# Kernel optimization log

Hardware: AMD Instinct MI355X
Metric: run time of the kernel (lower is better)

The kernel has to match this reference:

```python
import jax, jax.numpy as jnp
import numpy as np

B, D, R = 16384, 4096, 64       # batch tokens, embed_dim, low_rank_dimension
N_PART = 8                       # number of subspace partitions
P = R // N_PART                  # partition size = 8
N_SEL = 4                        # partitions selected per example


def setup_inputs() -> dict:
    key = jax.random.key(0)
    k1, k2, k3, k4 = jax.random.split(key, 4)
    base = jax.random.normal(k1, (B, D), dtype=jnp.float32)
    source = jax.random.normal(k2, (B, D), dtype=jnp.float32)
    # orthogonal low-rank rotation (torch.nn.utils.parametrizations.orthogonal)
    W, _ = jnp.linalg.qr(jax.random.normal(k3, (D, R), dtype=jnp.float32))  # [D, R], orthonormal cols
    subspaces = jax.random.randint(k4, (B, N_SEL), 0, N_PART)               # partition ids per example
    return {"base": base, "source": source, "W": W, "subspaces": subspaces}


def reference(base, source, W, subspaces):
    # rotate into low-rank space: [B, R]
    rotated_base = base @ W
    rotated_source = source @ W
    diff = rotated_source - rotated_base

    # per-example selected rotated-space indices (contiguous partitions of size P)
    # idx[b] = concat over selected partitions of [p*P, p*P+P)
    idx = (subspaces[:, :, None] * P + jnp.arange(P)).reshape(B, N_SEL * P)  # [B, N_SEL*P]

    # Selecting columns of diff and matching rows of W.T, then matmul, is
    # equivalent to masking unselected rotated dims to zero and doing one GEMM.
    mask = jnp.zeros((B, R), dtype=diff.dtype).at[jnp.arange(B)[:, None], idx].set(1.0)
    output = base + (diff * mask) @ W.T  # [B, D]
    return output.astype(base.dtype)
```

## Files before the change

kernel.cpp:

```cpp
#include <hip/hip_runtime.h>


#define D_DIM 4096
#define R_DIM 64
#define BM    32
#define WAVESTG 16384
#define OFF_RM  65536
#define SMEM_BYTES 70144

typedef short bf16vec8 __attribute__((ext_vector_type(8)));
typedef float f32x4v  __attribute__((ext_vector_type(4)));

__device__ __forceinline__ unsigned int f2bf_u(float f) {
  unsigned int u = __builtin_bit_cast(unsigned int, f);
  return (u + 0x7fffu + ((u >> 16) & 1u)) >> 16;
}
__device__ __forceinline__ unsigned int pack2bf(float a, float b) {
  return f2bf_u(a) | (f2bf_u(b) << 16);
}
__device__ __forceinline__ void async_ld16(const void* g, void* l) {
  __builtin_amdgcn_global_load_lds(
      (const __attribute__((address_space(1))) void*)g,
      (__attribute__((address_space(3))) void*)l, 16, 0, 0);
}

__global__ __launch_bounds__(256)
void lrri_prep(const float* __restrict__ W, unsigned short* __restrict__ Wt,
               unsigned short* __restrict__ Wb) {
  const int idx = blockIdx.x * blockDim.x + threadIdx.x;
  const int k = idx >> 4;
  const int j = (idx & 15) * 4;
  float4 w = *(const float4*)(W + (size_t)k * R_DIM + j);
  ushort4 p;
  p.x = (unsigned short)f2bf_u(w.x);
  p.y = (unsigned short)f2bf_u(w.y);
  p.z = (unsigned short)f2bf_u(w.z);
  p.w = (unsigned short)f2bf_u(w.w);
  *(ushort4*)(Wb + (size_t)k * R_DIM + j) = p;
  Wt[(size_t)(j + 0) * D_DIM + k] = p.x;
  Wt[(size_t)(j + 1) * D_DIM + k] = p.y;
  Wt[(size_t)(j + 2) * D_DIM + k] = p.z;
  Wt[(size_t)(j + 3) * D_DIM + k] = p.w;
}

template<bool USE_WS>
__global__ __launch_bounds__(256, 2)
void lrri_fused(const float* __restrict__ base, const float* __restrict__ srcp,
                const float* __restrict__ W, const int* __restrict__ subs,
                const unsigned short* __restrict__ Wt_bf,
                const unsigned short* __restrict__ Wb_bf,
                float* __restrict__ out)
{
  __shared__ __align__(16) unsigned char smem[SMEM_BYTES];
  const int tid  = threadIdx.x;
  const int wave = tid >> 6;
  const int lane = tid & 63;
  const int l4   = lane & 15;
  const int g    = lane >> 4;
  const int rh   = wave >> 1;
  const int kh   = wave & 1;
  const long rowbase = (long)blockIdx.x * BM;
  const long rowg    = rowbase + rh * 16;
  unsigned char* wbuf = smem + wave * WAVESTG;
  const int off1 = (blockIdx.x * 7) & 31;
  const int off2 = (blockIdx.x * 5) & 15;

  f32x4v acc[4];
  #pragma unroll
  for (int t = 0; t < 4; ++t) acc[t] = (f32x4v){0.f, 0.f, 0.f, 0.f};

  auto stage = [&](int p, int c) {
    const int chc = (c + off1) & 31;
    const int kb = kh * 2048 + chc * 64;
    unsigned char* buf = wbuf + p * 8192;
    #pragma unroll
    for (int i = 0; i < 4; ++i) {
      const int  r  = i * 4 + g;
      const unsigned cb = ((unsigned)(l4 * 16)) ^ ((unsigned)(r & 7) << 4);
      const long goff = (rowg + r) * (long)D_DIM + kb + (cb >> 2);
      async_ld16(base + goff, buf + i * 1024);
      async_ld16(srcp + goff, buf + 4096 + i * 1024);
    }
  };

  auto compute = [&](int p, int c) {
    const int chc = (c + off1) & 31;
    const int kb = kh * 2048 + chc * 64;
    const unsigned char* buf = wbuf + p * 8192;
    uint4 af[2];
    #pragma unroll
    for (int s = 0; s < 2; ++s) {
      const unsigned x = (unsigned)(l4 & 7) << 4;
      const unsigned cb0 = ((unsigned)(s * 128 + g * 32 +  0)) ^ x;
      const unsigned cb1 = ((unsigned)(s * 128 + g * 32 + 16)) ^ x;
      float4 fb0 = *(const float4*)(buf + l4 * 256 + cb0);
      float4 fb1 = *(const float4*)(buf + l4 * 256 + cb1);
      float4 fs0 = *(const float4*)(buf + 4096 + l4 * 256 + cb0);
      float4 fs1 = *(const float4*)(buf + 4096 + l4 * 256 + cb1);
      af[s].x = pack2bf(fs0.x - fb0.x, fs0.y - fb0.y);
      af[s].y = pack2bf(fs0.z - fb0.z, fs0.w - fb0.w);
      af[s].z = pack2bf(fs1.x - fb1.x, fs1.y - fb1.y);
      af[s].w = pack2bf(fs1.z - fb1.z, fs1.w - fb1.w);
    }
    #pragma unroll
    for (int t = 0; t < 4; ++t) {
      #pragma unroll
      for (int s = 0; s < 2; ++s) {
        uint4 bfrag;
        if (USE_WS) {
          bfrag = *(const uint4*)(Wt_bf + (size_t)(t * 16 + l4) * D_DIM +
                                  kb + s * 32 + g * 8);
        } else {
          unsigned int pq[4];
          #pragma unroll
          for (int e2 = 0; e2 < 4; ++e2) {
            float wa = W[(size_t)(kb + s * 32 + g * 8 + e2 * 2    ) * R_DIM + t * 16 + l4];
            float wb = W[(size_t)(kb + s * 32 + g * 8 + e2 * 2 + 1) * R_DIM + t * 16 + l4];
            pq[e2] = pack2bf(wa, wb);
          }
          bfrag.x = pq[0]; bfrag.y = pq[1]; bfrag.z = pq[2]; bfrag.w = pq[3];
        }
        acc[t] = __builtin_amdgcn_mfma_f32_16x16x32_bf16(
            __builtin_bit_cast(bf16vec8, af[s]),
            __builtin_bit_cast(bf16vec8, bfrag), acc[t], 0, 0, 0);
      }
    }
  };

  stage(0, 0);
  #pragma unroll 1
  for (int c = 0; c < 31; ++c) {
    stage((c + 1) & 1, c + 1);
    compute(c & 1, c);
  }
  compute(1, 31);

  {
    float* part = (float*)wbuf;
    #pragma unroll
    for (int t = 0; t < 4; ++t)
      #pragma unroll
      for (int i = 0; i < 4; ++i)
        part[(g * 4 + i) * 72 + t * 16 + l4] = acc[t][i];
  }
  __syncthreads();

  {
    const int row = tid >> 3, jg = tid & 7;
    const int lr  = row & 15;
    const float* pa = (const float*)(smem + ((row >> 4) * 2 + 0) * WAVESTG);
    const float* pb = (const float*)(smem + ((row >> 4) * 2 + 1) * WAVESTG);
    int4 sb = *(const int4*)(subs + (rowbase + row) * 4);
    unsigned mbits = (1u << sb.x) | (1u << sb.y) | (1u << sb.z) | (1u << sb.w);
    unsigned short v[8];
    #pragma unroll
    for (int jj = 0; jj < 8; ++jj) {
      const int j = jg * 8 + jj;
      float sum = pa[lr * 72 + j] + pb[lr * 72 + j];
      v[jj] = ((mbits >> (j >> 3)) & 1u) ? (unsigned short)f2bf_u(sum)
                                         : (unsigned short)0;
    }
    uint4 pk;
    pk.x = (unsigned)v[0] | ((unsigned)v[1] << 16);
    pk.y = (unsigned)v[2] | ((unsigned)v[3] << 16);
    pk.z = (unsigned)v[4] | ((unsigned)v[5] << 16);
    pk.w = (unsigned)v[6] | ((unsigned)v[7] << 16);
    *(uint4*)(smem + OFF_RM + row * 144 + jg * 16) = pk;
  }
  __syncthreads();

  uint4 a2[2][2];
  #pragma unroll
  for (int m = 0; m < 2; ++m)
    #pragma unroll
    for (int s = 0; s < 2; ++s)
      a2[m][s] = *(const uint4*)(smem + OFF_RM + (m * 16 + l4) * 144 +
                                 s * 64 + g * 16);
  float* cbuf = (float*)wbuf;
  #pragma unroll 1
  for (int grp = 0; grp < 16; ++grp) {
    const int ga = (grp + off2) & 15;
    const int cbase = wave * 1024 + ga * 64;
    float4 bb[8];
    #pragma unroll
    for (int v2 = 0; v2 < 8; ++v2) {
      const int r = g + v2 * 4;
      bb[v2] = *(const float4*)(base + (rowbase + r) * D_DIM + cbase + l4 * 4);
    }
    f32x4v a[2][4];
    #pragma unroll
    for (int m = 0; m < 2; ++m)
      #pragma unroll
      for (int t = 0; t < 4; ++t) a[m][t] = (f32x4v){0.f, 0.f, 0.f, 0.f};
    #pragma unroll
    for (int t = 0; t < 4; ++t) {
      #pragma unroll
      for (int s = 0; s < 2; ++s) {
        uint4 bfrag;
        if (USE_WS) {
          bfrag = *(const uint4*)(Wb_bf + (size_t)(cbase + t * 16 + l4) * R_DIM +
                                  s * 32 + g * 8);
        } else {
          const float* wp = W + (size_t)(cbase + t * 16 + l4) * R_DIM + s * 32 + g * 8;
          float4 wa = *(const float4*)(wp);
          float4 wb2 = *(const float4*)(wp + 4);
          bfrag.x = pack2bf(wa.x, wa.y); bfrag.y = pack2bf(wa.z, wa.w);
          bfrag.z = pack2bf(wb2.x, wb2.y); bfrag.w = pack2bf(wb2.z, wb2.w);
        }
        #pragma unroll
        for (int m = 0; m < 2; ++m)
          a[m][t] = __builtin_amdgcn_mfma_f32_16x16x32_bf16(
              __builtin_bit_cast(bf16vec8, a2[m][s]),
              __builtin_bit_cast(bf16vec8, bfrag), a[m][t], 0, 0, 0);
      }
    }
    #pragma unroll
    for (int m = 0; m < 2; ++m)
      #pragma unroll
      for (int t = 0; t < 4; ++t)
        #pragma unroll
        for (int i = 0; i < 4; ++i)
          cbuf[(m * 16 + g * 4 + i) * 72 + t * 16 + l4] = a[m][t][i];
    #pragma unroll
    for (int v2 = 0; v2 < 8; ++v2) {
      const int r = g + v2 * 4;
      f32x4v cv = *(const f32x4v*)(cbuf + r * 72 + l4 * 4);
      float4 o;
      o.x = cv[0] + bb[v2].x;
      o.y = cv[1] + bb[v2].y;
      o.z = cv[2] + bb[v2].z;
      o.w = cv[3] + bb[v2].w;
      *(float4*)(out + (rowbase + r) * D_DIM + cbase + l4 * 4) = o;
    }
  }
}

extern "C" void kernel_launch(void* const* d_in, const int* in_sizes, int n_in,
                              void* d_out, int out_size, void* d_ws, size_t ws_size,
                              hipStream_t stream) {
  const float* base = (const float*)d_in[0];
  const float* srcp = (const float*)d_in[1];
  const float* W    = (const float*)d_in[2];
  const int*   subs = (const int*)d_in[3];
  float* out = (float*)d_out;

  const int nblocks = 16384 / BM;
  const size_t wbytes = (size_t)2 * R_DIM * D_DIM * sizeof(unsigned short);
  if (d_ws && ws_size >= wbytes) {
    unsigned short* Wt = (unsigned short*)d_ws;
    unsigned short* Wb = Wt + (size_t)R_DIM * D_DIM;
    lrri_prep<<<256, 256, 0, stream>>>(W, Wt, Wb);
    lrri_fused<true><<<nblocks, 256, 0, stream>>>(base, srcp, W, subs, Wt, Wb, out);
  } else {
    lrri_fused<false><<<nblocks, 256, 0, stream>>>(base, srcp, W, subs, nullptr, nullptr, out);
  }
}
```

Baseline: 231.0 us.

## Stage W tiles in LDS and deepen async prefetch with explicit vmcnt waits

Halves the per-chunk column width so each wave keeps two chunks in flight, and issues the next chunk's loads right after computing the current one. Explicit s_waitcnt vmcnt(8) plus sched barriers replace the compiler's implicit full waits. The bf16 W fragments now go through LDS via async global-to-LDS loads along with base and source, instead of per-MFMA global loads. The goal is to hide HBM latency on this bandwidth-bound kernel, at the cost of more loop iterations and hand-tuned wait counts that could race if the count is wrong.

```diff
diff --git a/kernel.cpp b/kernel.cpp
--- a/kernel.cpp
+++ b/kernel.cpp
@@ -10,6 +10,12 @@
 
 typedef short bf16vec8 __attribute__((ext_vector_type(8)));
 typedef float f32x4v  __attribute__((ext_vector_type(4)));
+
+#define VMWAIT(N)                                              \
+  do {                                                         \
+    asm volatile("s_waitcnt vmcnt(" #N ")" ::: "memory");      \
+    __builtin_amdgcn_sched_barrier(0);                         \
+  } while (0)
 
 __device__ __forceinline__ unsigned int f2bf_u(float f) {
   unsigned int u = __builtin_bit_cast(unsigned int, f);
@@ -62,78 +68,121 @@
   const long rowbase = (long)blockIdx.x * BM;
   const long rowg    = rowbase + rh * 16;
   unsigned char* wbuf = smem + wave * WAVESTG;
-  const int off1 = (blockIdx.x * 7) & 31;
+  const int off1 = (blockIdx.x * 7) & 63;
   const int off2 = (blockIdx.x * 5) & 15;
 
   f32x4v acc[4];
   #pragma unroll
   for (int t = 0; t < 4; ++t) acc[t] = (f32x4v){0.f, 0.f, 0.f, 0.f};
 
-  auto stage = [&](int p, int c) {
-    const int chc = (c + off1) & 31;
-    const int kb = kh * 2048 + chc * 64;
-    unsigned char* buf = wbuf + p * 8192;
-    #pragma unroll
-    for (int i = 0; i < 4; ++i) {
-      const int  r  = i * 4 + g;
-      const unsigned cb = ((unsigned)(l4 * 16)) ^ ((unsigned)(r & 7) << 4);
-      const long goff = (rowg + r) * (long)D_DIM + kb + (cb >> 2);
-      async_ld16(base + goff, buf + i * 1024);
-      async_ld16(srcp + goff, buf + 4096 + i * 1024);
+  auto stage = [&](int c) {
+    const int ch = (c + off1) & 63;
+    unsigned char* buf = wbuf + (c & 1) * 8192;
+    const long colf = kh * 2048 + ch * 32;
+    #pragma unroll
+    for (int q = 0; q < 2; ++q) {
+      const int r = q * 8 + (lane >> 3);
+      const unsigned b = ((unsigned)((lane & 7) * 16)) ^ ((unsigned)(r & 7) << 4);
+      const long goff = (rowg + r) * (long)D_DIM + colf + (b >> 2);
+      async_ld16(base + goff, buf + q * 1024);
+    }
+    #pragma unroll
+    for (int q = 0; q < 2; ++q) {
+      const int r = q * 8 + (lane >> 3);
+      const unsigned b = ((unsigned)((lane & 7) * 16)) ^ ((unsigned)(r & 7) << 4);
+      const long goff = (rowg + r) * (long)D_DIM + colf + (b >> 2);
+      async_ld16(srcp + goff, buf + 2048 + q * 1024);
+    }
+    #pragma unroll
+    for (int q = 0; q < 4; ++q) {
+      const int j = q * 16 + (lane >> 2);
+      const unsigned kb = ((unsigned)((lane & 3) * 16)) ^ ((unsigned)(j & 3) << 4);
+      const char* src = (const char*)Wt_bf + (size_t)j * (D_DIM * 2) +
+                        colf * 2 + kb;
+      async_ld16(src, buf + 4096 + q * 1024);
     }
   };
 
-  auto compute = [&](int p, int c) {
-    const int chc = (c + off1) & 31;
-    const int kb = kh * 2048 + chc * 64;
-    const unsigned char* buf = wbuf + p * 8192;
-    uint4 af[2];
-    #pragma unroll
-    for (int s = 0; s < 2; ++s) {
-      const unsigned x = (unsigned)(l4 & 7) << 4;
-      const unsigned cb0 = ((unsigned)(s * 128 + g * 32 +  0)) ^ x;
-      const unsigned cb1 = ((unsigned)(s * 128 + g * 32 + 16)) ^ x;
-      float4 fb0 = *(const float4*)(buf + l4 * 256 + cb0);
-      float4 fb1 = *(const float4*)(buf + l4 * 256 + cb1);
-      float4 fs0 = *(const float4*)(buf + 4096 + l4 * 256 + cb0);
-      float4 fs1 = *(const float4*)(buf + 4096 + l4 * 256 + cb1);
-      af[s].x = pack2bf(fs0.x - fb0.x, fs0.y - fb0.y);
-      af[s].y = pack2bf(fs0.z - fb0.z, fs0.w - fb0.w);
-      af[s].z = pack2bf(fs1.x - fb1.x, fs1.y - fb1.y);
-      af[s].w = pack2bf(fs1.z - fb1.z, fs1.w - fb1.w);
-    }
+  auto compute = [&](int c) {
+    const unsigned char* buf = wbuf + (c & 1) * 8192;
+    const unsigned sw = (unsigned)((l4 & 7) << 4);
+    const unsigned c0 = ((unsigned)(g * 32)) ^ sw;
+    const unsigned c1 = ((unsigned)(g * 32 + 16)) ^ sw;
+    float4 fb0 = *(const float4*)(buf + l4 * 128 + c0);
+    float4 fb1 = *(const float4*)(buf + l4 * 128 + c1);
+    float4 fs0 = *(const float4*)(buf + 2048 + l4 * 128 + c0);
+    float4 fs1 = *(const float4*)(buf + 2048 + l4 * 128 + c1);
+    uint4 af;
+    af.x = pack2bf(fs0.x - fb0.x, fs0.y - fb0.y);
+    af.y = pack2bf(fs0.z - fb0.z, fs0.w - fb0.w);
+    af.z = pack2bf(fs1.x - fb1.x, fs1.y - fb1.y);
+    af.w = pack2bf(fs1.z - fb1.z, fs1.w - fb1.w);
+    const unsigned wsl = ((unsigned)(g * 16)) ^ ((unsigned)(l4 & 3) << 4);
     #pragma unroll
     for (int t = 0; t < 4; ++t) {
-      #pragma unroll
-      for (int s = 0; s < 2; ++s) {
-        uint4 bfrag;
-        if (USE_WS) {
-          bfrag = *(const uint4*)(Wt_bf + (size_t)(t * 16 + l4) * D_DIM +
-                                  kb + s * 32 + g * 8);
-        } else {
-          unsigned int pq[4];
-          #pragma unroll
-          for (int e2 = 0; e2 < 4; ++e2) {
-            float wa = W[(size_t)(kb + s * 32 + g * 8 + e2 * 2    ) * R_DIM + t * 16 + l4];
-            float wb = W[(size_t)(kb + s * 32 + g * 8 + e2 * 2 + 1) * R_DIM + t * 16 + l4];
-            pq[e2] = pack2bf(wa, wb);
-          }
-          bfrag.x = pq[0]; bfrag.y = pq[1]; bfrag.z = pq[2]; bfrag.w = pq[3];
+      uint4 wf = *(const uint4*)(buf + 4096 + (t * 16 + l4) * 64 + wsl);
+      acc[t] = __builtin_amdgcn_mfma_f32_16x16x32_bf16(
+          __builtin_bit_cast(bf16vec8, af),
+          __builtin_bit_cast(bf16vec8, wf), acc[t], 0, 0, 0);
+    }
+  };
+
+  if constexpr (USE_WS) {
+    stage(0); stage(1);
+    #pragma unroll 1
+    for (int c = 0; c < 62; ++c) {
+      VMWAIT(8);
+      compute(c);
+      __builtin_amdgcn_sched_barrier(0);
+      stage(c + 2);
+    }
+    VMWAIT(8);
+    compute(62);
+    VMWAIT(0);
+    compute(63);
+  } else {
+    #pragma unroll 1
+    for (int c = 0; c < 64; ++c) {
+      const int ch = (c + off1) & 63;
+      unsigned char* buf = wbuf + (c & 1) * 8192;
+      const long colf = kh * 2048 + ch * 32;
+      #pragma unroll
+      for (int q = 0; q < 2; ++q) {
+        const int r = q * 8 + (lane >> 3);
+        const unsigned b = ((unsigned)((lane & 7) * 16)) ^ ((unsigned)(r & 7) << 4);
+        const long goff = (rowg + r) * (long)D_DIM + colf + (b >> 2);
+        async_ld16(base + goff, buf + q * 1024);
+        async_ld16(srcp + goff, buf + 2048 + q * 1024);
+      }
+      VMWAIT(0);
+      const unsigned sw = (unsigned)((l4 & 7) << 4);
+      const unsigned c0 = ((unsigned)(g * 32)) ^ sw;
+      const unsigned c1 = ((unsigned)(g * 32 + 16)) ^ sw;
+      float4 fb0 = *(const float4*)(buf + l4 * 128 + c0);
+      float4 fb1 = *(const float4*)(buf + l4 * 128 + c1);
+      float4 fs0 = *(const float4*)(buf + 2048 + l4 * 128 + c0);
+      float4 fs1 = *(const float4*)(buf + 2048 + l4 * 128 + c1);
+      uint4 af;
+      af.x = pack2bf(fs0.x - fb0.x, fs0.y - fb0.y);
+      af.y = pack2bf(fs0.z - fb0.z, fs0.w - fb0.w);
+      af.z = pack2bf(fs1.x - fb1.x, fs1.y - fb1.y);
+      af.w = pack2bf(fs1.z - fb1.z, fs1.w - fb1.w);
+      #pragma unroll
+      for (int t = 0; t < 4; ++t) {
+        unsigned int pq[4];
+        #pragma unroll
+        for (int e2 = 0; e2 < 4; ++e2) {
+          float wa = W[(size_t)(colf + g * 8 + e2 * 2    ) * R_DIM + t * 16 + l4];
+          float wb = W[(size_t)(colf + g * 8 + e2 * 2 + 1) * R_DIM + t * 16 + l4];
+          pq[e2] = pack2bf(wa, wb);
         }
+        uint4 wf; wf.x = pq[0]; wf.y = pq[1]; wf.z = pq[2]; wf.w = pq[3];
         acc[t] = __builtin_amdgcn_mfma_f32_16x16x32_bf16(
-            __builtin_bit_cast(bf16vec8, af[s]),
-            __builtin_bit_cast(bf16vec8, bfrag), acc[t], 0, 0, 0);
+            __builtin_bit_cast(bf16vec8, af),
+            __builtin_bit_cast(bf16vec8, wf), acc[t], 0, 0, 0);
       }
     }
-  };
-
-  stage(0, 0);
-  #pragma unroll 1
-  for (int c = 0; c < 31; ++c) {
-    stage((c + 1) & 1, c + 1);
-    compute(c & 1, c);
-  }
-  compute(1, 31);
+  }
 
   {
     float* part = (float*)wbuf;
```

New measurement: 227.2 us, median of 2. About the same (-1.6%).

## Double row tile to 64 with 512-thread blocks and swizzled tile order

Applied to the files above, without the earlier changes.

Each block now processes 64 rows with 8 waves. In the output phase, each wave takes one 16-row quarter and one half of the columns instead of all 32 rows over a quarter of the columns. Block indices are remapped so that adjacent blocks touch distant row tiles. LDS use doubles to about 140KB, so only one block fits per CU. This trades occupancy for larger blocks and fewer reloads of the W fragment per row.

```diff
diff --git a/kernel.cpp b/kernel.cpp
--- a/kernel.cpp
+++ b/kernel.cpp
@@ -3,10 +3,10 @@
 
 #define D_DIM 4096
 #define R_DIM 64
-#define BM    32
+#define BM    64
 #define WAVESTG 16384
-#define OFF_RM  65536
-#define SMEM_BYTES 70144
+#define OFF_RM  131072
+#define SMEM_BYTES 140288
 
 typedef short bf16vec8 __attribute__((ext_vector_type(8)));
 typedef float f32x4v  __attribute__((ext_vector_type(4)));
@@ -44,7 +44,7 @@
 }
 
 template<bool USE_WS>
-__global__ __launch_bounds__(256, 2)
+__global__ __launch_bounds__(512, 1)
 void lrri_fused(const float* __restrict__ base, const float* __restrict__ srcp,
                 const float* __restrict__ W, const int* __restrict__ subs,
                 const unsigned short* __restrict__ Wt_bf,
@@ -57,13 +57,14 @@
   const int lane = tid & 63;
   const int l4   = lane & 15;
   const int g    = lane >> 4;
-  const int rh   = wave >> 1;
+  const int rq   = wave >> 1;
   const int kh   = wave & 1;
-  const long rowbase = (long)blockIdx.x * BM;
-  const long rowg    = rowbase + rh * 16;
+  const int tile = (blockIdx.x & 7) * 32 + (blockIdx.x >> 3);
+  const long rowbase = (long)tile * BM;
+  const long rowg    = rowbase + rq * 16;
   unsigned char* wbuf = smem + wave * WAVESTG;
-  const int off1 = (blockIdx.x * 7) & 31;
-  const int off2 = (blockIdx.x * 5) & 15;
+  const int off1 = (tile * 7) & 31;
+  const int off2 = (tile * 5) & 31;
 
   f32x4v acc[4];
   #pragma unroll
@@ -169,29 +170,25 @@
   }
   __syncthreads();
 
-  uint4 a2[2][2];
+  uint4 a2[2];
   #pragma unroll
-  for (int m = 0; m < 2; ++m)
-    #pragma unroll
-    for (int s = 0; s < 2; ++s)
-      a2[m][s] = *(const uint4*)(smem + OFF_RM + (m * 16 + l4) * 144 +
-                                 s * 64 + g * 16);
+  for (int s = 0; s < 2; ++s)
+    a2[s] = *(const uint4*)(smem + OFF_RM + (rq * 16 + l4) * 144 +
+                            s * 64 + g * 16);
   float* cbuf = (float*)wbuf;
   #pragma unroll 1
-  for (int grp = 0; grp < 16; ++grp) {
-    const int ga = (grp + off2) & 15;
-    const int cbase = wave * 1024 + ga * 64;
-    float4 bb[8];
-    #pragma unroll
-    for (int v2 = 0; v2 < 8; ++v2) {
-      const int r = g + v2 * 4;
+  for (int grp = 0; grp < 32; ++grp) {
+    const int ga = (grp + off2) & 31;
+    const int cbase = kh * 2048 + ga * 64;
+    float4 bb[4];
+    #pragma unroll
+    for (int v2 = 0; v2 < 4; ++v2) {
+      const int r = rq * 16 + g + v2 * 4;
       bb[v2] = *(const float4*)(base + (rowbase + r) * D_DIM + cbase + l4 * 4);
     }
-    f32x4v a[2][4];
-    #pragma unroll
-    for (int m = 0; m < 2; ++m)
-      #pragma unroll
-      for (int t = 0; t < 4; ++t) a[m][t] = (f32x4v){0.f, 0.f, 0.f, 0.f};
+    f32x4v a[4];
+    #pragma unroll
+    for (int t = 0; t < 4; ++t) a[t] = (f32x4v){0.f, 0.f, 0.f, 0.f};
     #pragma unroll
     for (int t = 0; t < 4; ++t) {
       #pragma unroll
@@ -207,24 +204,20 @@
           bfrag.x = pack2bf(wa.x, wa.y); bfrag.y = pack2bf(wa.z, wa.w);
           bfrag.z = pack2bf(wb2.x, wb2.y); bfrag.w = pack2bf(wb2.z, wb2.w);
         }
-        #pragma unroll
-        for (int m = 0; m < 2; ++m)
-          a[m][t] = __builtin_amdgcn_mfma_f32_16x16x32_bf16(
-              __builtin_bit_cast(bf16vec8, a2[m][s]),
-              __builtin_bit_cast(bf16vec8, bfrag), a[m][t], 0, 0, 0);
+        a[t] = __builtin_amdgcn_mfma_f32_16x16x32_bf16(
+            __builtin_bit_cast(bf16vec8, a2[s]),
+            __builtin_bit_cast(bf16vec8, bfrag), a[t], 0, 0, 0);
       }
     }
     #pragma unroll
-    for (int m = 0; m < 2; ++m)
-      #pragma unroll
-      for (int t = 0; t < 4; ++t)
-        #pragma unroll
-        for (int i = 0; i < 4; ++i)
-          cbuf[(m * 16 + g * 4 + i) * 72 + t * 16 + l4] = a[m][t][i];
-    #pragma unroll
-    for (int v2 = 0; v2 < 8; ++v2) {
-      const int r = g + v2 * 4;
-      f32x4v cv = *(const f32x4v*)(cbuf + r * 72 + l4 * 4);
+    for (int t = 0; t < 4; ++t)
+      #pragma unroll
+      for (int i = 0; i < 4; ++i)
+        cbuf[(g * 4 + i) * 72 + t * 16 + l4] = a[t][i];
+    #pragma unroll
+    for (int v2 = 0; v2 < 4; ++v2) {
+      const int r = rq * 16 + g + v2 * 4;
+      f32x4v cv = *(const f32x4v*)(cbuf + (g + v2 * 4) * 72 + l4 * 4);
       float4 o;
       o.x = cv[0] + bb[v2].x;
       o.y = cv[1] + bb[v2].y;
@@ -250,8 +243,8 @@
     unsigned short* Wt = (unsigned short*)d_ws;
     unsigned short* Wb = Wt + (size_t)R_DIM * D_DIM;
     lrri_prep<<<256, 256, 0, stream>>>(W, Wt, Wb);
-    lrri_fused<true><<<nblocks, 256, 0, stream>>>(base, srcp, W, subs, Wt, Wb, out);
+    lrri_fused<true><<<nblocks, 512, 0, stream>>>(base, srcp, W, subs, Wt, Wb, out);
   } else {
-    lrri_fused<false><<<nblocks, 256, 0, stream>>>(base, srcp, W, subs, nullptr, nullptr, out);
-  }
-}
+    lrri_fused<false><<<nblocks, 512, 0, stream>>>(base, srcp, W, subs, nullptr, nullptr, out);
+  }
+}
```

Measured after the change: 250.1 us. 8.3% more time.
